# Kernel optimization log

Hardware: AMD Instinct MI355X
Metric: run time of the kernel (lower is better)

## Reference

```python
import jax, jax.numpy as jnp
import numpy as np

B, N, DIM = 4, 16384, 256
H, D, G = 8, 64, 32  # heads, dim_head, slice_num; inner = H*D = 512


def setup_inputs() -> dict:
    key = jax.random.key(0)
    ks = jax.random.split(key, 12)
    inner = H * D
    s = lambda fan_in: 1.0 / np.sqrt(fan_in)
    inp = {
        "x": jax.random.normal(ks[0], (B, N, DIM), jnp.float32),
        # weights stored (in, out) so forward is x @ W + b
        "Wfx": jax.random.uniform(ks[1], (DIM, inner), jnp.float32, -s(DIM), s(DIM)),
        "bfx": jnp.zeros((inner,), jnp.float32),
        "Wx": jax.random.uniform(ks[2], (DIM, inner), jnp.float32, -s(DIM), s(DIM)),
        "bx": jnp.zeros((inner,), jnp.float32),
        "Wslice": jnp.linalg.qr(jax.random.normal(ks[3], (D, G), jnp.float32))[0],  # orthogonal init
        "bslice": jnp.zeros((G,), jnp.float32),
        "temperature": jnp.full((1, H, 1, 1), 0.5, jnp.float32),
        "Wq": jax.random.uniform(ks[4], (D, D), jnp.float32, -s(D), s(D)),
        "Wk": jax.random.uniform(ks[5], (D, D), jnp.float32, -s(D), s(D)),
        "Wv": jax.random.uniform(ks[6], (D, D), jnp.float32, -s(D), s(D)),
        "Wout": jax.random.uniform(ks[7], (inner, DIM), jnp.float32, -s(inner), s(inner)),
        "bout": jnp.zeros((DIM,), jnp.float32),
    }
    return inp


def reference(x, Wfx, bfx, Wx, bx, Wslice, bslice, temperature, Wq, Wk, Wv, Wout, bout):
    b, n, _ = x.shape
    # projections -> [B, H, N, D]
    fx_mid = (x @ Wfx + bfx).reshape(b, n, H, D).transpose(0, 2, 1, 3)
    x_mid = (x @ Wx + bx).reshape(b, n, H, D).transpose(0, 2, 1, 3)
    # soft slice assignment: [B, H, N, G]
    slice_logits = (x_mid @ Wslice + bslice) / temperature
    slice_weights = jax.nn.softmax(slice_logits, axis=-1)
    slice_norm = slice_weights.sum(axis=2)  # [B, H, G]
    # soft pooling to G slice tokens: [B, H, G, D]
    slice_token = jnp.einsum("bhnd,bhng->bhgd", fx_mid, slice_weights)
    slice_token = slice_token / (slice_norm[..., None] + 1e-5)
    # tiny attention over G tokens
    q = slice_token @ Wq
    k = slice_token @ Wk
    v = slice_token @ Wv
    scores = jnp.einsum("bhgd,bhkd->bhgk", q, k) / jnp.sqrt(jnp.asarray(D, q.dtype))
    attn = jax.nn.softmax(scores, axis=-1)
    out_slice = jnp.einsum("bhgk,bhkd->bhgd", attn, v)
    # scatter back to N points: [B, H, N, D] -> [B, N, H*D]
    out_x = jnp.einsum("bhgd,bhng->bhnd", out_slice, slice_weights)
    out_x = out_x.transpose(0, 2, 1, 3).reshape(b, n, H * D)
    return out_x @ Wout + bout
```

## Files before the change

### kernel.cpp

```cpp
#include <hip/hip_runtime.h>


typedef unsigned short u16;
typedef __attribute__((ext_vector_type(8))) unsigned short ushort8v;
typedef __attribute__((ext_vector_type(4))) unsigned short ushort4v;
typedef __attribute__((ext_vector_type(8))) short short8v;
typedef __attribute__((ext_vector_type(4))) float f32x4;

constexpr int Nc = 16384;
constexpr int BNc = 65536;

__device__ inline float b2f(u16 v) {
    union { unsigned int u; float f; } t; t.u = ((unsigned int)v) << 16; return t.f;
}
__device__ inline u16 f2b(float f) {
    union { float f; unsigned int u; } t; t.f = f;
    unsigned int u = t.u;
    return (u16)((u + 0x7fffu + ((u >> 16) & 1u)) >> 16);
}

__global__ __launch_bounds__(256) void k0_fold(
    const float* __restrict__ Wx, const float* __restrict__ Wslice,
    const float* __restrict__ bx, const float* __restrict__ bslice,
    u16* __restrict__ WxsT, float* __restrict__ bxs)
{
    int blk = blockIdx.x, tid = threadIdx.x;
    int h = tid >> 5, g = tid & 31;
    if (blk < 256) {
        int k = blk;
        float acc = 0.f;
        for (int d = 0; d < 64; d++)
            acc += Wx[k * 512 + h * 64 + d] * Wslice[d * 32 + g];
        WxsT[tid * 256 + k] = f2b(acc);
    } else {
        float acc = 0.f;
        for (int d = 0; d < 64; d++)
            acc += bx[h * 64 + d] * Wslice[d * 32 + g];
        bxs[tid] = acc + bslice[g];
    }
}

__global__ __launch_bounds__(256) void kprep_wfx(const float* __restrict__ Wfx,
                                                 u16* __restrict__ WfxT)
{
    int n = blockIdx.x, k = threadIdx.x;
    WfxT[n * 256 + k] = f2b(Wfx[k * 512 + n]);
}

__global__ __launch_bounds__(256) void kfrag(const u16* __restrict__ Ball,
                                             u16* __restrict__ Bf)
{
    int g = blockIdx.x * 256 + threadIdx.x;
    int pair = g >> 6, lane = g & 63;
    int t = pair >> 3, c = pair & 7;
    int n = t * 16 + (lane & 15);
    int k = c * 32 + (lane >> 4) * 8;
    ushort8v v = *(const ushort8v*)(Ball + (size_t)n * 256 + k);
    *(ushort8v*)(Bf + (size_t)((c * 48 + t) * 64 + lane) * 8) = v;
}

__global__ __launch_bounds__(256, 3) void kproj(
    const float* __restrict__ x, const u16* __restrict__ Bf,
    const float* __restrict__ bfx, const float* __restrict__ bxs,
    const float* __restrict__ temp,
    u16* __restrict__ fxT, u16* __restrict__ swb, u16* __restrict__ swT)
{
    __shared__ u16 Bs[48 * 512];
    int tid = threadIdx.x;
    int wave = tid >> 6, lane = tid & 63;
    int lm = lane & 15, quad = lane >> 4;
    int wr = wave & 1, wc = wave >> 1;
    int row0 = blockIdx.x * 32;
    int arow = row0 + wr * 16 + lm;

    const float* Aptr = x + (size_t)arow * 256 + quad * 8;

    f32x4 acc[24] = {};

    f32x4 a0 = *(const f32x4*)(Aptr);
    f32x4 a1 = *(const f32x4*)(Aptr + 4);

    for (int c = 0; c < 8; c++) {
        const u16* src = Bf + (size_t)c * 24576 + (size_t)(wave * 12) * 512 + lane * 8;
#pragma unroll
        for (int i = 0; i < 12; i++) {
            ushort8v v = *(const ushort8v*)(src + i * 512);
            *(ushort8v*)&Bs[(wave * 12 + i) * 512 + lane * 8] = v;
        }
        ushort8v au;
#pragma unroll
        for (int j = 0; j < 4; j++) { au[j] = f2b(a0[j]); au[4 + j] = f2b(a1[j]); }
        short8v af = (short8v&)au;
        if (c < 7) {
            a0 = *(const f32x4*)(Aptr + c * 32 + 32);
            a1 = *(const f32x4*)(Aptr + c * 32 + 36);
        }
        __syncthreads();
#pragma unroll
        for (int j = 0; j < 24; j++) {
            short8v bf = *(short8v*)&Bs[(wc * 24 + j) * 512 + lane * 8];
            acc[j] = __builtin_amdgcn_mfma_f32_16x16x32_bf16(af, bf, acc[j], 0, 0, 0);
        }
        __syncthreads();
    }

    int nbase = row0 + wr * 16 + quad * 4;
    int nfx = wc ? 8 : 24;
#pragma unroll
    for (int j = 0; j < 24; j++) {
        if (j < nfx) {
            int cc = (wc * 24 + j) * 16 + lm;
            float bv = bfx[cc];
            ushort4v o;
#pragma unroll
            for (int r = 0; r < 4; r++) o[r] = f2b(acc[j][r] + bv);
            *(ushort4v*)(fxT + (size_t)cc * 65536 + nbase) = o;
        }
    }

    if (wc == 1) {
        int b = row0 >> 14;
        int nlbase = (row0 & 16383) + wr * 16 + quad * 4;
#pragma unroll
        for (int h = 0; h < 8; h++) {
            float it = 1.0f / temp[h];
            float bv0 = bxs[h * 32 + lm];
            float bv1 = bxs[h * 32 + 16 + lm];
            f32x4 A0 = acc[8 + 2 * h];
            f32x4 A1 = acc[9 + 2 * h];
            ushort4v p0, p1;
#pragma unroll
            for (int r = 0; r < 4; r++) {
                float v0 = (A0[r] + bv0) * it;
                float v1 = (A1[r] + bv1) * it;
                float m = fmaxf(v0, v1);
                m = fmaxf(m, __shfl_xor(m, 1));
                m = fmaxf(m, __shfl_xor(m, 2));
                m = fmaxf(m, __shfl_xor(m, 4));
                m = fmaxf(m, __shfl_xor(m, 8));
                float e0 = __expf(v0 - m), e1 = __expf(v1 - m);
                float s = e0 + e1;
                s += __shfl_xor(s, 1);
                s += __shfl_xor(s, 2);
                s += __shfl_xor(s, 4);
                s += __shfl_xor(s, 8);
                float rs = 1.0f / s;
                float w0 = e0 * rs, w1 = e1 * rs;
                int row = row0 + wr * 16 + quad * 4 + r;
                swb[(size_t)row * 256 + h * 32 + lm] = f2b(w0);
                swb[(size_t)row * 256 + h * 32 + 16 + lm] = f2b(w1);
                p0[r] = f2b(w0); p1[r] = f2b(w1);
            }
            size_t gbase = (size_t)((b * 8 + h) * 32);
            *(ushort4v*)(swT + (gbase + lm) * 16384 + nlbase) = p0;
            *(ushort4v*)(swT + (gbase + 16 + lm) * 16384 + nlbase) = p1;
        }
    }
}

__global__ __launch_bounds__(256, 4) void kout(
    const u16* __restrict__ swb, const u16* __restrict__ ZTf,
    const float* __restrict__ bout, float* __restrict__ out)
{
    __shared__ u16 Bs[16 * 512];
    int tid = threadIdx.x;
    int wave = tid >> 6, lane = tid & 63;
    int lm = lane & 15, quad = lane >> 4;
    int row0 = blockIdx.x * 64;

    const u16* Abase = swb + (size_t)(row0 + wave * 16 + lm) * 256 + quad * 8;
    const u16* Zb    = ZTf + (size_t)(row0 >> 14) * 65536;

    f32x4 acc[16] = {};
    short8v af = *(const short8v*)(Abase);
    for (int c = 0; c < 8; c++) {
        const u16* src = Zb + (size_t)c * 8192 + (size_t)(wave * 4) * 512 + lane * 8;
#pragma unroll
        for (int i = 0; i < 4; i++) {
            ushort8v v = *(const ushort8v*)(src + i * 512);
            *(ushort8v*)&Bs[(wave * 4 + i) * 512 + lane * 8] = v;
        }
        short8v a_cur = af;
        if (c < 7) af = *(const short8v*)(Abase + c * 32 + 32);
        __syncthreads();
#pragma unroll
        for (int j = 0; j < 16; j++) {
            short8v bf = *(short8v*)&Bs[j * 512 + lane * 8];
            acc[j] = __builtin_amdgcn_mfma_f32_16x16x32_bf16(a_cur, bf, acc[j], 0, 0, 0);
        }
        __syncthreads();
    }
#pragma unroll
    for (int j = 0; j < 16; j++) {
        int cc = j * 16 + lm;
        float bv = bout[cc];
#pragma unroll
        for (int r = 0; r < 4; r++)
            out[(size_t)(row0 + wave * 16 + quad * 4 + r) * 256 + cc] = acc[j][r] + bv;
    }
}

__global__ __launch_bounds__(256) void k4_token_mfma(
    const u16* __restrict__ swT, const u16* __restrict__ fxT,
    float* __restrict__ token_part, float* __restrict__ norm_part)
{
    int bh = blockIdx.x, ky = blockIdx.y;
    int b = bh >> 3, h = bh & 7;
    int tid = threadIdx.x, wave = tid >> 6, lane = tid & 63;
    int lm = lane & 15, quad = lane >> 4;
    int mt = wave & 1, dp = wave >> 1;
    const u16* Ar = swT + ((size_t)(bh * 32 + mt * 16 + lm)) * 16384 + ky * 512 + quad * 8;
    const u16* Br0 = fxT + ((size_t)(h * 64 + dp * 32 + lm)) * 65536
                     + (size_t)b * 16384 + ky * 512 + quad * 8;
    const u16* Br1 = Br0 + (size_t)16 * 65536;
    f32x4 acc0 = {}, acc1 = {};
    float nacc = 0.f;
#pragma unroll
    for (int kk = 0; kk < 16; kk++) {
        short8v af = *(const short8v*)(Ar + kk * 32);
        short8v b0 = *(const short8v*)(Br0 + kk * 32);
        short8v b1 = *(const short8v*)(Br1 + kk * 32);
        acc0 = __builtin_amdgcn_mfma_f32_16x16x32_bf16(af, b0, acc0, 0, 0, 0);
        acc1 = __builtin_amdgcn_mfma_f32_16x16x32_bf16(af, b1, acc1, 0, 0, 0);
        if (dp == 0) {
            ushort8v au = (ushort8v&)af;
#pragma unroll
            for (int j = 0; j < 8; j++) nacc += b2f(au[j]);
        }
    }
    float* tp = token_part + ((size_t)(ky * 32 + bh)) * 2048;
#pragma unroll
    for (int r = 0; r < 4; r++) {
        int g = mt * 16 + quad * 4 + r;
        tp[g * 64 + dp * 32 + lm] = acc0[r];
        tp[g * 64 + dp * 32 + 16 + lm] = acc1[r];
    }
    if (dp == 0) {
        nacc += __shfl_xor(nacc, 16);
        nacc += __shfl_xor(nacc, 32);
        if (lane < 16)
            norm_part[(ky * 32 + bh) * 32 + mt * 16 + lm] = nacc;
    }
}

__global__ __launch_bounds__(256) void k4b_reduce(
    const float* __restrict__ tp, const float* __restrict__ np,
    float* __restrict__ tl)
{
    int t = blockIdx.x * 256 + threadIdx.x;
    int bh = t >> 11, e = t & 2047, g = e >> 6;
    float ts = 0.f, ns = 0.f;
    for (int ch = 0; ch < 32; ch++) {
        ts += tp[((size_t)(ch * 32 + bh)) * 2048 + e];
        ns += np[(ch * 32 + bh) * 32 + g];
    }
    tl[t] = ts / (ns + 1e-5f);
}

__global__ __launch_bounds__(256) void k5_attn(
    const float* __restrict__ tlg,
    const float* __restrict__ Wq, const float* __restrict__ Wk, const float* __restrict__ Wv,
    float* __restrict__ out_slice)
{
    __shared__ float tl[32][64];
    __shared__ float ql[32][64], kl[32][64], vl[32][64];
    __shared__ float sl[32][33];
    int bh = blockIdx.x, tid = threadIdx.x;
    const float* tk = tlg + (size_t)bh * 2048;

#pragma unroll
    for (int j = 0; j < 8; j++) {
        int idx = j * 256 + tid;
        tl[idx >> 6][idx & 63] = tk[idx];
    }
    __syncthreads();
#pragma unroll
    for (int j = 0; j < 8; j++) {
        int idx = j * 256 + tid;
        int g = idx >> 6, d = idx & 63;
        float aq = 0.f, ak = 0.f, av = 0.f;
        for (int e = 0; e < 64; e++) {
            float t = tl[g][e];
            aq += t * Wq[e * 64 + d];
            ak += t * Wk[e * 64 + d];
            av += t * Wv[e * 64 + d];
        }
        ql[g][d] = aq; kl[g][d] = ak; vl[g][d] = av;
    }
    __syncthreads();
#pragma unroll
    for (int j = 0; j < 4; j++) {
        int idx = j * 256 + tid;
        int gq = idx >> 5, gk = idx & 31;
        float s = 0.f;
        for (int d = 0; d < 64; d++) s += ql[gq][d] * kl[gk][d];
        sl[gq][gk] = s * 0.125f;
    }
    __syncthreads();
    if (tid < 32) {
        float m = -1e30f;
        for (int k2 = 0; k2 < 32; k2++) m = fmaxf(m, sl[tid][k2]);
        float s = 0.f;
        for (int k2 = 0; k2 < 32; k2++) { float e = __expf(sl[tid][k2] - m); sl[tid][k2] = e; s += e; }
        float r = 1.0f / s;
        for (int k2 = 0; k2 < 32; k2++) sl[tid][k2] *= r;
    }
    __syncthreads();
#pragma unroll
    for (int j = 0; j < 8; j++) {
        int idx = j * 256 + tid;
        int g = idx >> 6, d = idx & 63;
        float a = 0.f;
        for (int k2 = 0; k2 < 32; k2++) a += sl[g][k2] * vl[k2][d];
        out_slice[(size_t)bh * 2048 + idx] = a;
    }
}

__global__ __launch_bounds__(256) void kZ(
    const float* __restrict__ os, const float* __restrict__ Wout,
    u16* __restrict__ ZTf)
{
    int b = blockIdx.x, cb = blockIdx.y;
    int t = threadIdx.x;
    int c = cb * 16 + (t & 15), kq = t >> 4;
    int tile = c >> 4, lm = c & 15;
    for (int k = kq * 16; k < kq * 16 + 16; k++) {
        int h = k >> 5, g = k & 31;
        const float* osr = os + ((size_t)(b * 8 + h)) * 2048 + g * 64;
        float acc = 0.f;
        for (int d = 0; d < 64; d++)
            acc += osr[d] * Wout[(h * 64 + d) * 256 + c];
        int ch = k >> 5, quad = (k >> 3) & 3, jj = k & 7;
        int lane = quad * 16 + lm;
        ZTf[((size_t)((b * 8 + ch) * 16 + tile)) * 512 + lane * 8 + jj] = f2b(acc);
    }
}

extern "C" void kernel_launch(void* const* d_in, const int* in_sizes, int n_in,
                              void* d_out, int out_size, void* d_ws, size_t ws_size,
                              hipStream_t stream)
{
    const float* x      = (const float*)d_in[0];
    const float* Wfx    = (const float*)d_in[1];
    const float* bfx    = (const float*)d_in[2];
    const float* Wx     = (const float*)d_in[3];
    const float* bx     = (const float*)d_in[4];
    const float* Wslice = (const float*)d_in[5];
    const float* bslice = (const float*)d_in[6];
    const float* temp   = (const float*)d_in[7];
    const float* Wq     = (const float*)d_in[8];
    const float* Wk     = (const float*)d_in[9];
    const float* Wv     = (const float*)d_in[10];
    const float* Wout   = (const float*)d_in[11];
    const float* bout   = (const float*)d_in[12];

    char* ws = (char*)d_ws;
    size_t off = 0;
    auto alloc = [&](size_t bytes) {
        void* p = ws + off;
        off = (off + bytes + 255) & ~(size_t)255;
        return p;
    };
    u16*   fxT   = (u16*)  alloc((size_t)512 * BNc * 2);
    u16*   swb   = (u16*)  alloc((size_t)BNc * 256 * 2);
    u16*   swT   = (u16*)  alloc((size_t)1024 * Nc * 2);
    float* tp    = (float*)alloc((size_t)1024 * 2048 * 4);
    float* np    = (float*)alloc(32768 * 4);
    float* tl    = (float*)alloc(65536 * 4);
    float* osl   = (float*)alloc(65536 * 4);
    u16*   ZTf   = (u16*)  alloc(4 * 65536 * 2);
    u16*   Ball  = (u16*)  alloc((size_t)768 * 256 * 2);
    u16*   Bfrg  = (u16*)  alloc((size_t)768 * 256 * 2);
    float* bxs   = (float*)alloc(256 * 4);

    u16* WfxT = Ball;
    u16* WxsT = Ball + (size_t)512 * 256;

    k0_fold<<<257, 256, 0, stream>>>(Wx, Wslice, bx, bslice, WxsT, bxs);
    kprep_wfx<<<512, 256, 0, stream>>>(Wfx, WfxT);
    kfrag<<<96, 256, 0, stream>>>(Ball, Bfrg);

    kproj<<<2048, 256, 0, stream>>>(x, Bfrg, bfx, bxs, temp, fxT, swb, swT);

    k4_token_mfma<<<dim3(32, 32), 256, 0, stream>>>(swT, fxT, tp, np);
    k4b_reduce<<<256, 256, 0, stream>>>(tp, np, tl);
    k5_attn<<<32, 256, 0, stream>>>(tl, Wq, Wk, Wv, osl);
    kZ<<<dim3(4, 16), 256, 0, stream>>>(osl, Wout, ZTf);

    kout<<<1024, 256, 0, stream>>>(swb, ZTf, bout, (float*)d_out);
}
```

Baseline: 391.4 us.

## Split projection across column groups with double-buffered LDS, stage token GEMM in LDS

The projection kernel now runs on a 2D grid that splits the 768 output columns into two halves. Each block holds 12 accumulators instead of 24, which allows higher occupancy, and it double-buffers the weight fragments in LDS through direct global-to-LDS loads so the next chunk's fetch overlaps the current MFMAs. Softmax work is redistributed across waves of the second column group. The token-pooling kernel stages swizzled A/B tiles into LDS via global_load_lds and doubles the K-split count (64 chunks of 256). The reduce kernel now sums more partials, and the x reads are duplicated across the two column groups.

New measurement: 376.0 us. 3.9% less time.

```diff
diff --git a/kernel.cpp b/kernel.cpp
--- a/kernel.cpp
+++ b/kernel.cpp
@@ -59,33 +59,44 @@
     *(ushort8v*)(Bf + (size_t)((c * 48 + t) * 64 + lane) * 8) = v;
 }
 
-__global__ __launch_bounds__(256, 3) void kproj(
+__global__ __launch_bounds__(256, 4) void kproj(
     const float* __restrict__ x, const u16* __restrict__ Bf,
     const float* __restrict__ bfx, const float* __restrict__ bxs,
     const float* __restrict__ temp,
     u16* __restrict__ fxT, u16* __restrict__ swb, u16* __restrict__ swT)
 {
-    __shared__ u16 Bs[48 * 512];
+    __shared__ u16 Bs[2][12288];
     int tid = threadIdx.x;
     int wave = tid >> 6, lane = tid & 63;
     int lm = lane & 15, quad = lane >> 4;
     int wr = wave & 1, wc = wave >> 1;
+    int cg = blockIdx.y;
     int row0 = blockIdx.x * 32;
     int arow = row0 + wr * 16 + lm;
 
     const float* Aptr = x + (size_t)arow * 256 + quad * 8;
-
-    f32x4 acc[24] = {};
-
+    const u16* BfW = Bf + (size_t)cg * 12288 + (size_t)(wave * 6) * 512 + lane * 8;
+
+    f32x4 acc[12] = {};
     f32x4 a0 = *(const f32x4*)(Aptr);
     f32x4 a1 = *(const f32x4*)(Aptr + 4);
 
+#pragma unroll
+    for (int i = 0; i < 6; i++)
+        __builtin_amdgcn_global_load_lds((const uint32_t*)(BfW + i * 512),
+                                         (uint32_t*)(&Bs[0][(wave * 6 + i) * 512]),
+                                         16, 0, 0);
+    __syncthreads();
+
+    int cur = 0;
     for (int c = 0; c < 8; c++) {
-        const u16* src = Bf + (size_t)c * 24576 + (size_t)(wave * 12) * 512 + lane * 8;
-#pragma unroll
-        for (int i = 0; i < 12; i++) {
-            ushort8v v = *(const ushort8v*)(src + i * 512);
-            *(ushort8v*)&Bs[(wave * 12 + i) * 512 + lane * 8] = v;
+        if (c < 7) {
+            const u16* src = BfW + (size_t)(c + 1) * 24576;
+            u16* dst = &Bs[cur ^ 1][(wave * 6) * 512];
+#pragma unroll
+            for (int i = 0; i < 6; i++)
+                __builtin_amdgcn_global_load_lds((const uint32_t*)(src + i * 512),
+                                                 (uint32_t*)(dst + i * 512), 16, 0, 0);
         }
         ushort8v au;
 #pragma unroll
@@ -95,21 +106,22 @@
             a0 = *(const f32x4*)(Aptr + c * 32 + 32);
             a1 = *(const f32x4*)(Aptr + c * 32 + 36);
         }
+#pragma unroll
+        for (int j = 0; j < 12; j++) {
+            short8v bf = *(short8v*)&Bs[cur][(wc * 12 + j) * 512 + lane * 8];
+            acc[j] = __builtin_amdgcn_mfma_f32_16x16x32_bf16(af, bf, acc[j], 0, 0, 0);
+        }
         __syncthreads();
-#pragma unroll
-        for (int j = 0; j < 24; j++) {
-            short8v bf = *(short8v*)&Bs[(wc * 24 + j) * 512 + lane * 8];
-            acc[j] = __builtin_amdgcn_mfma_f32_16x16x32_bf16(af, bf, acc[j], 0, 0, 0);
-        }
-        __syncthreads();
+        cur ^= 1;
     }
 
     int nbase = row0 + wr * 16 + quad * 4;
-    int nfx = wc ? 8 : 24;
-#pragma unroll
-    for (int j = 0; j < 24; j++) {
+    int tbase = cg * 24 + wc * 12;
+    int nfx = (cg == 0) ? 12 : (wc == 0 ? 8 : 0);
+#pragma unroll
+    for (int j = 0; j < 12; j++) {
         if (j < nfx) {
-            int cc = (wc * 24 + j) * 16 + lm;
+            int cc = (tbase + j) * 16 + lm;
             float bv = bfx[cc];
             ushort4v o;
 #pragma unroll
@@ -118,42 +130,46 @@
         }
     }
 
-    if (wc == 1) {
+    if (cg == 1) {
         int b = row0 >> 14;
         int nlbase = (row0 & 16383) + wr * 16 + quad * 4;
-#pragma unroll
-        for (int h = 0; h < 8; h++) {
-            float it = 1.0f / temp[h];
-            float bv0 = bxs[h * 32 + lm];
-            float bv1 = bxs[h * 32 + 16 + lm];
-            f32x4 A0 = acc[8 + 2 * h];
-            f32x4 A1 = acc[9 + 2 * h];
-            ushort4v p0, p1;
-#pragma unroll
-            for (int r = 0; r < 4; r++) {
-                float v0 = (A0[r] + bv0) * it;
-                float v1 = (A1[r] + bv1) * it;
-                float m = fmaxf(v0, v1);
-                m = fmaxf(m, __shfl_xor(m, 1));
-                m = fmaxf(m, __shfl_xor(m, 2));
-                m = fmaxf(m, __shfl_xor(m, 4));
-                m = fmaxf(m, __shfl_xor(m, 8));
-                float e0 = __expf(v0 - m), e1 = __expf(v1 - m);
-                float s = e0 + e1;
-                s += __shfl_xor(s, 1);
-                s += __shfl_xor(s, 2);
-                s += __shfl_xor(s, 4);
-                s += __shfl_xor(s, 8);
-                float rs = 1.0f / s;
-                float w0 = e0 * rs, w1 = e1 * rs;
-                int row = row0 + wr * 16 + quad * 4 + r;
-                swb[(size_t)row * 256 + h * 32 + lm] = f2b(w0);
-                swb[(size_t)row * 256 + h * 32 + 16 + lm] = f2b(w1);
-                p0[r] = f2b(w0); p1[r] = f2b(w1);
+        int nh = wc ? 6 : 2, h0 = wc ? 2 : 0, jb = wc ? 0 : 8;
+#pragma unroll
+        for (int hh = 0; hh < 6; hh++) {
+            if (hh < nh) {
+                int h = h0 + hh;
+                float it = 1.0f / temp[h];
+                float bv0 = bxs[h * 32 + lm];
+                float bv1 = bxs[h * 32 + 16 + lm];
+                f32x4 A0 = acc[jb + 2 * hh];
+                f32x4 A1 = acc[jb + 2 * hh + 1];
+                ushort4v p0, p1;
+#pragma unroll
+                for (int r = 0; r < 4; r++) {
+                    float v0 = (A0[r] + bv0) * it;
+                    float v1 = (A1[r] + bv1) * it;
+                    float m = fmaxf(v0, v1);
+                    m = fmaxf(m, __shfl_xor(m, 1));
+                    m = fmaxf(m, __shfl_xor(m, 2));
+                    m = fmaxf(m, __shfl_xor(m, 4));
+                    m = fmaxf(m, __shfl_xor(m, 8));
+                    float e0 = __expf(v0 - m), e1 = __expf(v1 - m);
+                    float s = e0 + e1;
+                    s += __shfl_xor(s, 1);
+                    s += __shfl_xor(s, 2);
+                    s += __shfl_xor(s, 4);
+                    s += __shfl_xor(s, 8);
+                    float rs = 1.0f / s;
+                    float w0 = e0 * rs, w1 = e1 * rs;
+                    int row = row0 + wr * 16 + quad * 4 + r;
+                    swb[(size_t)row * 256 + h * 32 + lm] = f2b(w0);
+                    swb[(size_t)row * 256 + h * 32 + 16 + lm] = f2b(w1);
+                    p0[r] = f2b(w0); p1[r] = f2b(w1);
+                }
+                size_t gbase = (size_t)((b * 8 + h) * 32);
+                *(ushort4v*)(swT + (gbase + lm) * 16384 + nlbase) = p0;
+                *(ushort4v*)(swT + (gbase + 16 + lm) * 16384 + nlbase) = p1;
             }
-            size_t gbase = (size_t)((b * 8 + h) * 32);
-            *(ushort4v*)(swT + (gbase + lm) * 16384 + nlbase) = p0;
-            *(ushort4v*)(swT + (gbase + 16 + lm) * 16384 + nlbase) = p1;
         }
     }
 }
@@ -200,26 +216,57 @@
     }
 }
 
-__global__ __launch_bounds__(256) void k4_token_mfma(
+__global__ __launch_bounds__(256, 4) void k4_token_mfma(
     const u16* __restrict__ swT, const u16* __restrict__ fxT,
     float* __restrict__ token_part, float* __restrict__ norm_part)
 {
+    __shared__ u16 As[32 * 256];
+    __shared__ u16 Bs_[64 * 256];
     int bh = blockIdx.x, ky = blockIdx.y;
     int b = bh >> 3, h = bh & 7;
     int tid = threadIdx.x, wave = tid >> 6, lane = tid & 63;
     int lm = lane & 15, quad = lane >> 4;
     int mt = wave & 1, dp = wave >> 1;
-    const u16* Ar = swT + ((size_t)(bh * 32 + mt * 16 + lm)) * 16384 + ky * 512 + quad * 8;
-    const u16* Br0 = fxT + ((size_t)(h * 64 + dp * 32 + lm)) * 65536
-                     + (size_t)b * 16384 + ky * 512 + quad * 8;
-    const u16* Br1 = Br0 + (size_t)16 * 65536;
+    int lh = lane >> 5, lb = lane & 31;
+
+#pragma unroll
+    for (int i = 0; i < 4; i++) {
+        int s = wave * 4 + i;
+        int r = 2 * s + lh;
+        int sw = ((lb * 16) ^ ((r & 7) << 4)) >> 1;
+        const u16* src = swT + (size_t)(bh * 32 + r) * 16384 + ky * 256 + sw;
+        __builtin_amdgcn_global_load_lds((const uint32_t*)src,
+                                         (uint32_t*)(&As[s * 512]), 16, 0, 0);
+    }
+#pragma unroll
+    for (int i = 0; i < 8; i++) {
+        int s = wave * 8 + i;
+        int r = 2 * s + lh;
+        int sw = ((lb * 16) ^ ((r & 7) << 4)) >> 1;
+        const u16* src = fxT + (size_t)(h * 64 + r) * 65536 + (size_t)b * 16384
+                         + ky * 256 + sw;
+        __builtin_amdgcn_global_load_lds((const uint32_t*)src,
+                                         (uint32_t*)(&Bs_[s * 512]), 16, 0, 0);
+    }
+    __syncthreads();
+
+    int rA = mt * 16 + lm;
+    int rB0 = dp * 32 + lm, rB1 = rB0 + 16;
+    const char* Ab  = (const char*)As  + rA  * 512;
+    const char* Bb0 = (const char*)Bs_ + rB0 * 512;
+    const char* Bb1 = (const char*)Bs_ + rB1 * 512;
+    int swA  = (rA  & 7) << 4;
+    int swB0 = (rB0 & 7) << 4;
+    int swB1 = (rB1 & 7) << 4;
+
     f32x4 acc0 = {}, acc1 = {};
     float nacc = 0.f;
 #pragma unroll
-    for (int kk = 0; kk < 16; kk++) {
-        short8v af = *(const short8v*)(Ar + kk * 32);
-        short8v b0 = *(const short8v*)(Br0 + kk * 32);
-        short8v b1 = *(const short8v*)(Br1 + kk * 32);
+    for (int kk = 0; kk < 8; kk++) {
+        int base = kk * 64 + quad * 16;
+        short8v af = *(const short8v*)(Ab  + (base ^ swA));
+        short8v b0 = *(const short8v*)(Bb0 + (base ^ swB0));
+        short8v b1 = *(const short8v*)(Bb1 + (base ^ swB1));
         acc0 = __builtin_amdgcn_mfma_f32_16x16x32_bf16(af, b0, acc0, 0, 0, 0);
         acc1 = __builtin_amdgcn_mfma_f32_16x16x32_bf16(af, b1, acc1, 0, 0, 0);
         if (dp == 0) {
@@ -250,7 +297,7 @@
     int t = blockIdx.x * 256 + threadIdx.x;
     int bh = t >> 11, e = t & 2047, g = e >> 6;
     float ts = 0.f, ns = 0.f;
-    for (int ch = 0; ch < 32; ch++) {
+    for (int ch = 0; ch < 64; ch++) {
         ts += tp[((size_t)(ch * 32 + bh)) * 2048 + e];
         ns += np[(ch * 32 + bh) * 32 + g];
     }
@@ -364,8 +411,8 @@
     u16*   fxT   = (u16*)  alloc((size_t)512 * BNc * 2);
     u16*   swb   = (u16*)  alloc((size_t)BNc * 256 * 2);
     u16*   swT   = (u16*)  alloc((size_t)1024 * Nc * 2);
-    float* tp    = (float*)alloc((size_t)1024 * 2048 * 4);
-    float* np    = (float*)alloc(32768 * 4);
+    float* tp    = (float*)alloc((size_t)2048 * 2048 * 4);
+    float* np    = (float*)alloc((size_t)2048 * 32 * 4);
     float* tl    = (float*)alloc(65536 * 4);
     float* osl   = (float*)alloc(65536 * 4);
     u16*   ZTf   = (u16*)  alloc(4 * 65536 * 2);
@@ -380,9 +427,9 @@
     kprep_wfx<<<512, 256, 0, stream>>>(Wfx, WfxT);
     kfrag<<<96, 256, 0, stream>>>(Ball, Bfrg);
 
-    kproj<<<2048, 256, 0, stream>>>(x, Bfrg, bfx, bxs, temp, fxT, swb, swT);
-
-    k4_token_mfma<<<dim3(32, 32), 256, 0, stream>>>(swT, fxT, tp, np);
+    kproj<<<dim3(2048, 2), 256, 0, stream>>>(x, Bfrg, bfx, bxs, temp, fxT, swb, swT);
+
+    k4_token_mfma<<<dim3(32, 64), 256, 0, stream>>>(swT, fxT, tp, np);
     k4b_reduce<<<256, 256, 0, stream>>>(tp, np, tl);
     k5_attn<<<32, 256, 0, stream>>>(tl, Wq, Wk, Wv, osl);
     kZ<<<dim3(4, 16), 256, 0, stream>>>(osl, Wout, ZTf);
```
